# Performance work log

Measured on AMD Instinct MI355X. Metric: run time of the kernel, lower is better.

## Reference

```python
import jax, jax.numpy as jnp
import numpy as np
import math

B, S, D, H = 4, 1024, 1024, 16
DK = D // H


def setup_inputs() -> dict:
    key = jax.random.key(0)
    ks = jax.random.split(key, 13)
    s = 1.0 / math.sqrt(D)
    inp = {
        "query": jax.random.normal(ks[0], (B, S, D), jnp.float32),
        "key": jax.random.normal(ks[1], (B, S, D), jnp.float32),
        "value": jax.random.normal(ks[2], (B, S, D), jnp.float32),
        "mask": jax.random.randint(ks[3], (B, S, S), 0, 2, jnp.int32),
        "wq": jax.random.normal(ks[4], (D, D), jnp.float32) * s,
        "bq": jax.random.normal(ks[5], (D,), jnp.float32) * s,
        "wk": jax.random.normal(ks[6], (D, D), jnp.float32) * s,
        "bk": jax.random.normal(ks[7], (D,), jnp.float32) * s,
        "wv": jax.random.normal(ks[8], (D, D), jnp.float32) * s,
        "bv": jax.random.normal(ks[9], (D,), jnp.float32) * s,
        "wo": jax.random.normal(ks[10], (D, D), jnp.float32) * s,
        "bo": jax.random.normal(ks[11], (D,), jnp.float32) * s,
    }
    return inp


def reference(query, key, value, mask, wq, bq, wk, bk, wv, bv, wo, bo):
    # QKV projections, split into heads: [B,S,D] -> [B,H,S,DK]
    def proj(x, w, b):
        return (x @ w.T + b).reshape(B, S, H, DK).transpose(0, 2, 1, 3)

    q = proj(query, wq, bq)
    k = proj(key, wk, bk)
    v = proj(value, wv, bv)

    scores = jnp.einsum("bhqd,bhkd->bhqk", q, k) / math.sqrt(DK)
    scores = scores + mask[:, None, :, :].astype(scores.dtype) * (-1e9)
    p = jax.nn.softmax(scores, axis=-1)
    x = jnp.einsum("bhqk,bhkd->bhqd", p, v)
    x = x.transpose(0, 2, 1, 3).reshape(B, S, D)
    # output projection (dropout is identity in eval)
    return x @ wo.T + bo
```

## Files before the change

### kernel.cpp

```cpp
#include <hip/hip_runtime.h>
#include <hip/hip_bf16.h>


typedef __bf16 bf16x8 __attribute__((ext_vector_type(8)));
typedef float f32x4 __attribute__((ext_vector_type(4)));
typedef unsigned short us8 __attribute__((ext_vector_type(8)));
typedef unsigned short us4 __attribute__((ext_vector_type(4)));

#define MFMA(a, b, c) __builtin_amdgcn_mfma_f32_16x16x32_bf16(a, b, c, 0, 0, 0)
#define EXP2(x) __builtin_amdgcn_exp2f(x)

__device__ __forceinline__ unsigned short f2b(float f) {
  return __builtin_bit_cast(unsigned short, __float2bfloat16(f));
}
__device__ __forceinline__ float b2f(unsigned short u) {
  return __builtin_bit_cast(float, (unsigned)u << 16);
}
__device__ __forceinline__ unsigned cvtpk(float lo, float hi) {
  unsigned r;
  asm("v_cvt_pk_bf16_f32 %0, %1, %2" : "=v"(r) : "v"(lo), "v"(hi));
  return r;
}
__device__ __forceinline__ bf16x8 ldbf8(const unsigned short* p) {
  return __builtin_bit_cast(bf16x8, *reinterpret_cast<const us8*>(p));
}
__device__ __forceinline__ us8 cvt8(float4 a, float4 b) {
  us8 o;
  o[0] = f2b(a.x); o[1] = f2b(a.y); o[2] = f2b(a.z); o[3] = f2b(a.w);
  o[4] = f2b(b.x); o[5] = f2b(b.y); o[6] = f2b(b.z); o[7] = f2b(b.w);
  return o;
}
__device__ __forceinline__ void glds16(const void* g, void* l) {
  __builtin_amdgcn_global_load_lds(
      (const __attribute__((address_space(1))) unsigned int*)g,
      (__attribute__((address_space(3))) unsigned int*)l, 16, 0, 0);
}

__global__ __launch_bounds__(256)
void prep(const float* __restrict__ query, const float* __restrict__ key,
          const float* __restrict__ value, const float* __restrict__ wq,
          const float* __restrict__ wk, const float* __restrict__ wv,
          unsigned short* __restrict__ Abfq, unsigned short* __restrict__ Abfk,
          unsigned short* __restrict__ Abfv, unsigned short* __restrict__ Wb) {
  const int bid = blockIdx.x, tid = threadIdx.x;
  const float* src;
  unsigned short* dst;
  size_t off;
  if (bid < 1536) {
    const int widx = bid >> 9;
    src = (widx == 0) ? wq : (widx == 1) ? wk : wv;
    dst = Wb + (size_t)widx * 1048576;
    off = (size_t)(bid & 511) * 2048 + tid * 8;
  } else if (bid < 3584) {
    src = query; dst = Abfq; off = (size_t)(bid - 1536) * 2048 + tid * 8;
  } else if (bid < 5632) {
    src = key; dst = Abfk; off = (size_t)(bid - 3584) * 2048 + tid * 8;
  } else {
    src = value; dst = Abfv; off = (size_t)(bid - 5632) * 2048 + tid * 8;
  }
  const float4* p = reinterpret_cast<const float4*>(src + off);
  *reinterpret_cast<us8*>(dst + off) = cvt8(p[0], p[1]);
}

__global__ __launch_bounds__(256)
void maskcvt(const int* __restrict__ mask, unsigned short* __restrict__ Mf) {
  const int idx = blockIdx.x * 256 + threadIdx.x;
  const int wl = idx & 63, tile = idx >> 6;
  const int kt = tile & 63, qt = (tile >> 6) & 63, b = tile >> 12;
  const int lr = wl & 15, lg = wl >> 4;
  const int4 mv = *reinterpret_cast<const int4*>(
      mask + (size_t)(b * 1024 + qt * 16 + lr) * 1024 + kt * 16 + lg * 4);
  us4 o;
  o[0] = mv.x ? 0xCEACu : 0xC1C0u;
  o[1] = mv.y ? 0xCEACu : 0xC1C0u;
  o[2] = mv.z ? 0xCEACu : 0xC1C0u;
  o[3] = mv.w ? 0xCEACu : 0xC1C0u;
  *reinterpret_cast<us4*>(Mf + (size_t)idx * 4) = o;
}

__global__ __launch_bounds__(256)
void cvt_w(const float* __restrict__ src, unsigned short* __restrict__ dst) {
  const size_t off = (size_t)blockIdx.x * 2048 + threadIdx.x * 8;
  const float4* p = reinterpret_cast<const float4*>(src + off);
  *reinterpret_cast<us8*>(dst + off) = cvt8(p[0], p[1]);
}

__global__ __launch_bounds__(256, 4)
void gemm_proj(const unsigned short* __restrict__ Aq,
               const unsigned short* __restrict__ Ak,
               const unsigned short* __restrict__ Av_bf,
               const float* __restrict__ Av_f32,
               const unsigned short* __restrict__ Wb,
               const float* __restrict__ bq, const float* __restrict__ bk,
               const float* __restrict__ bv, unsigned short* __restrict__ Qb,
               unsigned short* __restrict__ Kf, unsigned short* __restrict__ Vf,
               float qscale) {
  constexpr int K = 1024, N = 1024;
  __shared__ __align__(16) unsigned short As[2][128 * 32];
  __shared__ __align__(16) unsigned short Bs[2][128 * 32];
  const int lid = blockIdx.x + (blockIdx.y << 5) + (blockIdx.z << 8);
  const int xcd = lid & 7, slot = lid >> 3;
  const int chunk = ((slot >> 3) << 3) + xcd;
  const int z = chunk >> 5;
  const int bm = (chunk & 31) * 128;
  const int bn = (slot & 7) * 128;

  const unsigned short* Abf = (z == 0) ? Aq : (z == 1) ? Ak : Av_bf;
  const bool f32path = (z == 2) && (Av_bf == nullptr);
  const unsigned short* Bw = Wb + (size_t)z * 1048576;
  const float* bias = (z == 0) ? bq : (z == 1) ? bk : bv;
  const int t = threadIdx.x;
  const int w = t >> 6, lane = t & 63, lr = lane & 15, lg = lane >> 4;
  const int wr = w >> 1, wc = w & 1;

#define SWZ(row) ((((row) ^ ((row) >> 2)) & 3) << 4)

  f32x4 acc[4][4];
#pragma unroll
  for (int m = 0; m < 4; ++m)
#pragma unroll
    for (int n = 0; n < 4; ++n) acc[m][n] = f32x4{0.f, 0.f, 0.f, 0.f};

  auto stageA = [&](int k0, int buf) {
#pragma unroll
    for (int it = 0; it < 2; ++it) {
      const int s = it * 256 + t, row = s >> 2, cb = (s & 3) * 16;
      const char* g = (const char*)Abf + ((size_t)(bm + row) * 1024 + k0) * 2 +
                      (cb ^ SWZ(row));
      char* l = (char*)&As[buf][0] + (it * 256 + w * 64) * 16;
      glds16(g, l);
    }
  };
  auto stageB = [&](int k0, int buf) {
#pragma unroll
    for (int it = 0; it < 2; ++it) {
      const int s = it * 256 + t, row = s >> 2, cb = (s & 3) * 16;
      const char* g = (const char*)Bw + ((size_t)(bn + row) * 1024 + k0) * 2 +
                      (cb ^ SWZ(row));
      char* l = (char*)&Bs[buf][0] + (it * 256 + w * 64) * 16;
      glds16(g, l);
    }
  };
#define STA8(buf, it, v)                                                       \
  {                                                                            \
    const int s_ = (it) * 256 + t, row_ = s_ >> 2, cb_ = (s_ & 3) * 16;        \
    *reinterpret_cast<us8*>((char*)&As[buf][0] + row_ * 64 +                   \
                            (cb_ ^ SWZ(row_))) = (v);                          \
  }

  if (f32path) {
#pragma unroll
    for (int it = 0; it < 2; ++it) {
      const int s = it * 256 + t, row = s >> 2, col = (s & 3) * 8;
      const float4* p =
          reinterpret_cast<const float4*>(Av_f32 + (size_t)(bm + row) * K + col);
      STA8(0, it, cvt8(p[0], p[1]));
    }
  } else {
    stageA(0, 0);
  }
  stageB(0, 0);
  __syncthreads();

  for (int c = 0; c < 32; ++c) {
    const int buf = c & 1;
    float4 fa[4];
    if (c < 31) {
      const int k1 = (c + 1) * 32;
      if (f32path) {
#pragma unroll
        for (int it = 0; it < 2; ++it) {
          const int s = it * 256 + t, row = s >> 2, col = (s & 3) * 8;
          const float4* p = reinterpret_cast<const float4*>(
              Av_f32 + (size_t)(bm + row) * K + k1 + col);
          fa[2 * it] = p[0];
          fa[2 * it + 1] = p[1];
        }
      } else {
        stageA(k1, buf ^ 1);
      }
      stageB(k1, buf ^ 1);
    }
    {
      bf16x8 af[4], bfr[4];
#pragma unroll
      for (int m = 0; m < 4; ++m) {
        const int row = wr * 64 + m * 16 + lr;
        af[m] = ldbf8((const unsigned short*)((char*)&As[buf][0] + row * 64 +
                                              ((lg * 16) ^ SWZ(row))));
      }
#pragma unroll
      for (int n = 0; n < 4; ++n) {
        const int row = wc * 64 + n * 16 + lr;
        bfr[n] = ldbf8((const unsigned short*)((char*)&Bs[buf][0] + row * 64 +
                                               ((lg * 16) ^ SWZ(row))));
      }
#pragma unroll
      for (int m = 0; m < 4; ++m)
#pragma unroll
        for (int n = 0; n < 4; ++n) acc[m][n] = MFMA(af[m], bfr[n], acc[m][n]);
    }
    if (c < 31 && f32path) {
#pragma unroll
      for (int it = 0; it < 2; ++it) STA8(buf ^ 1, it, cvt8(fa[2 * it], fa[2 * it + 1]));
    }
    __syncthreads();
  }
#undef STA8
#undef SWZ

#pragma unroll
  for (int m = 0; m < 4; ++m) {
    const int mr = bm + wr * 64 + m * 16 + lg * 4;
#pragma unroll
    for (int nt = 0; nt < 4; ++nt) {
      const int n = bn + wc * 64 + nt * 16 + lr;
      const float bb = bias[n];
      if (z == 0) {
#pragma unroll
        for (int r = 0; r < 4; ++r)
          Qb[(size_t)(mr + r) * N + n] = f2b((acc[m][nt][r] + bb) * qscale);
      } else if (z == 1) {
        const int b2 = mr >> 10, s0 = mr & 1023, hh = n >> 6, dd = n & 63;
        const size_t base = (size_t)(b2 * 16 + hh) * 65536 + (size_t)(dd >> 5) * 32768 +
                            (size_t)(s0 >> 4) * 512 +
                            (size_t)((s0 & 15) | (((dd >> 3) & 3) << 4)) * 8 + (dd & 7);
#pragma unroll
        for (int r = 0; r < 4; ++r) Kf[base + r * 8] = f2b(acc[m][nt][r] + bb);
      } else {
        const int b2 = mr >> 10, s0 = mr & 1023, hh = n >> 6, dd = n & 63;
        const size_t base = (size_t)(b2 * 16 + hh) * 65536 + (size_t)(s0 >> 5) * 2048 +
                            (size_t)(dd >> 4) * 512 +
                            (size_t)((dd & 15) | (((s0 >> 3) & 3) << 4)) * 8 + (s0 & 7);
        us4 pk;
#pragma unroll
        for (int r = 0; r < 4; ++r) pk[r] = f2b(acc[m][nt][r] + bb);
        *reinterpret_cast<us4*>(&Vf[base]) = pk;
      }
    }
  }
}

__global__ __launch_bounds__(256)
void gemm_out(const unsigned short* __restrict__ A, const unsigned short* __restrict__ Bw,
              const float* __restrict__ bias, float* __restrict__ Out) {
  constexpr int K = 1024, N = 1024;
  __shared__ __align__(16) unsigned short As[2][128 * 64];
  __shared__ __align__(16) unsigned short Bs[2][64 * 64];
  const int lid = blockIdx.x + (blockIdx.y << 5);
  const int xcd = lid & 7, slot = lid >> 3;
  const int chunk = ((slot >> 5) << 3) + xcd;
  const int pos = slot & 31;
  const int bm = ((chunk << 1) + (pos >> 4)) * 128;
  const int bn = (pos & 15) * 64;
  const int t = threadIdx.x;
  const int w = t >> 6, lane = t & 63, lr = lane & 15, lg = lane >> 4;
  const int wr = w >> 1, wc = w & 1;
  const int swzc = (lr & 7) << 4;

  f32x4 acc[4][2];
#pragma unroll
  for (int m = 0; m < 4; ++m)
#pragma unroll
    for (int n = 0; n < 2; ++n) acc[m][n] = f32x4{0.f, 0.f, 0.f, 0.f};

  auto stageA = [&](int k0, int buf) {
#pragma unroll
    for (int it = 0; it < 4; ++it) {
      const int s = it * 256 + t, row = s >> 3, cb = (s & 7) * 16;
      const char* g = (const char*)A + ((size_t)(bm + row) * 1024 + k0) * 2 +
                      (cb ^ ((row & 7) << 4));
      char* l = (char*)&As[buf][0] + (it * 256 + w * 64) * 16;
      glds16(g, l);
    }
  };
  auto stageB = [&](int k0, int buf) {
#pragma unroll
    for (int it = 0; it < 2; ++it) {
      const int s = it * 256 + t, row = s >> 3, cb = (s & 7) * 16;
      const char* g = (const char*)Bw + ((size_t)(bn + row) * 1024 + k0) * 2 +
                      (cb ^ ((row & 7) << 4));
      char* l = (char*)&Bs[buf][0] + (it * 256 + w * 64) * 16;
      glds16(g, l);
    }
  };

  stageA(0, 0);
  stageB(0, 0);
  __syncthreads();

  for (int c = 0; c < 16; ++c) {
    const int buf = c & 1;
    if (c < 15) {
      const int k1 = (c + 1) * 64;
      stageA(k1, buf ^ 1);
      stageB(k1, buf ^ 1);
    }
#pragma unroll
    for (int h2 = 0; h2 < 2; ++h2) {
      bf16x8 af[4], bfr[2];
#pragma unroll
      for (int m = 0; m < 4; ++m) {
        const int row = wr * 64 + m * 16 + lr;
        af[m] = ldbf8((const unsigned short*)((char*)&As[buf][0] + row * 128 +
                                              ((h2 * 64 + lg * 16) ^ swzc)));
      }
#pragma unroll
      for (int n = 0; n < 2; ++n) {
        const int row = wc * 32 + n * 16 + lr;
        bfr[n] = ldbf8((const unsigned short*)((char*)&Bs[buf][0] + row * 128 +
                                               ((h2 * 64 + lg * 16) ^ swzc)));
      }
#pragma unroll
      for (int m = 0; m < 4; ++m)
#pragma unroll
        for (int n = 0; n < 2; ++n) acc[m][n] = MFMA(af[m], bfr[n], acc[m][n]);
    }
    __syncthreads();
  }

#pragma unroll
  for (int m = 0; m < 4; ++m) {
    const int mr = bm + wr * 64 + m * 16 + lg * 4;
#pragma unroll
    for (int nt = 0; nt < 2; ++nt) {
      const int n = bn + wc * 32 + nt * 16 + lr;
      const float bb = bias[n];
#pragma unroll
      for (int r = 0; r < 4; ++r) Out[(size_t)(mr + r) * N + n] = acc[m][nt][r] + bb;
    }
  }
}

__global__ __launch_bounds__(256)
void attn_v6(const unsigned short* __restrict__ Qb,
             const unsigned short* __restrict__ Kf,
             const unsigned short* __restrict__ Vf,
             const unsigned short* __restrict__ Mf,
             unsigned short* __restrict__ ctx) {
  __shared__ __align__(16) unsigned short sP[4][16 * 64];
  const int lid = blockIdx.x + (blockIdx.y << 6);
  const int xcd = lid & 7, slot = lid >> 3;
  const int bh = ((slot >> 4) << 3) + xcd;
  const int qb = slot & 15;
  const int b = bh >> 4, h = bh & 15;
  const int t = threadIdx.x, w = t >> 6, wl = t & 63, lr = wl & 15, lg = wl >> 4;
  const int q0 = qb * 64 + w * 16;
  const int swz = (lr & 7) << 4;

  const unsigned short* qp = Qb + (size_t)(b * 1024 + q0 + lr) * 1024 + h * 64 + lg * 8;
  const bf16x8 bq0 = ldbf8(qp);
  const bf16x8 bq1 = ldbf8(qp + 32);

  const unsigned short* KfB = Kf + (size_t)bh * 65536;
  const unsigned short* VfB = Vf + (size_t)bh * 65536;
  const unsigned short* mfp = Mf + (size_t)((b * 64 + qb * 4 + w) * 64) * 256 + wl * 4;

  f32x4 O[4];
  float l_ = 0.f;
#pragma unroll
  for (int dt = 0; dt < 4; ++dt) O[dt] = f32x4{0.f, 0.f, 0.f, 0.f};
  unsigned short* sp = &sP[w][0];

  for (int kc = 0; kc < 16; ++kc) {
    bf16x8 ak[4][2];
#pragma unroll
    for (int t4 = 0; t4 < 4; ++t4) {
      ak[t4][0] = ldbf8(KfB + (size_t)(kc * 4 + t4) * 512 + wl * 8);
      ak[t4][1] = ldbf8(KfB + 32768 + (size_t)(kc * 4 + t4) * 512 + wl * 8);
    }
    us4 mk[4];
#pragma unroll
    for (int t4 = 0; t4 < 4; ++t4)
      mk[t4] = *reinterpret_cast<const us4*>(mfp + (size_t)(kc * 4 + t4) * 256);
    bf16x8 bv[2][4];
#pragma unroll
    for (int ks = 0; ks < 2; ++ks)
#pragma unroll
      for (int dt = 0; dt < 4; ++dt)
        bv[ks][dt] = ldbf8(VfB + (size_t)(kc * 2 + ks) * 2048 + dt * 512 + wl * 8);

    f32x4 sc[4];
    __builtin_amdgcn_s_setprio(1);
#pragma unroll
    for (int t4 = 0; t4 < 4; ++t4) {
      f32x4 a;
#pragma unroll
      for (int r = 0; r < 4; ++r) a[r] = b2f(mk[t4][r]);
      a = MFMA(ak[t4][0], bq0, a);
      a = MFMA(ak[t4][1], bq1, a);
      sc[t4] = a;
    }
    __builtin_amdgcn_s_setprio(0);

    float ps = 0.f;
#pragma unroll
    for (int t4 = 0; t4 < 4; ++t4) {
      const float e0 = EXP2(sc[t4][0]), e1 = EXP2(sc[t4][1]);
      const float e2 = EXP2(sc[t4][2]), e3 = EXP2(sc[t4][3]);
      ps += (e0 + e1) + (e2 + e3);
      uint2 pw;
      pw.x = cvtpk(e0, e1);
      pw.y = cvtpk(e2, e3);
      *reinterpret_cast<uint2*>((char*)sp + lr * 128 + ((t4 * 32 + lg * 8) ^ swz)) = pw;
    }
    ps += __shfl_xor(ps, 16);
    ps += __shfl_xor(ps, 32);
    l_ += ps;

    __builtin_amdgcn_s_setprio(1);
#pragma unroll
    for (int ks = 0; ks < 2; ++ks) {
      bf16x8 ap =
          ldbf8((const unsigned short*)((char*)sp + lr * 128 + ((ks * 64 + lg * 16) ^ swz)));
#pragma unroll
      for (int dt = 0; dt < 4; ++dt) O[dt] = MFMA(ap, bv[ks][dt], O[dt]);
    }
    __builtin_amdgcn_s_setprio(0);
  }

  float linv[4];
#pragma unroll
  for (int r = 0; r < 4; ++r) linv[r] = 1.0f / __shfl(l_, lg * 4 + r);
#pragma unroll
  for (int dt = 0; dt < 4; ++dt)
#pragma unroll
    for (int r = 0; r < 4; ++r)
      ctx[(size_t)(b * 1024 + q0 + lg * 4 + r) * 1024 + h * 64 + dt * 16 + lr] =
          f2b(O[dt][r] * linv[r]);
}

extern "C" void kernel_launch(void* const* d_in, const int* in_sizes, int n_in,
                              void* d_out, int out_size, void* d_ws, size_t ws_size,
                              hipStream_t stream) {
  const float* query = (const float*)d_in[0];
  const float* key   = (const float*)d_in[1];
  const float* value = (const float*)d_in[2];
  const int*   mask  = (const int*)d_in[3];
  const float* wq = (const float*)d_in[4];
  const float* bq = (const float*)d_in[5];
  const float* wk = (const float*)d_in[6];
  const float* bk = (const float*)d_in[7];
  const float* wv = (const float*)d_in[8];
  const float* bv = (const float*)d_in[9];
  const float* wo = (const float*)d_in[10];
  const float* bo = (const float*)d_in[11];
  float* out = (float*)d_out;

  const size_t SZ = (size_t)4096 * 1024;
  unsigned short* Qb   = (unsigned short*)d_ws;
  unsigned short* Kf   = Qb + SZ;
  unsigned short* Vf   = Kf + SZ;
  unsigned short* ctx  = Vf + SZ;
  unsigned short* Abfq = (unsigned short*)d_out;
  unsigned short* Wb   = Abfq + SZ;
  unsigned short* Mf   = (unsigned short*)d_out;
  unsigned short* Abfk = ctx;
  const bool big = ws_size >= (size_t)40 * 1024 * 1024;
  unsigned short* Abfv = big ? (ctx + SZ) : nullptr;
  unsigned short* Wob  = Vf;

  const float qscale = 0.125f * 1.4426950408889634f;
  dim3 blk(256);
  prep<<<big ? 7680 : 5632, blk, 0, stream>>>(query, key, value, wq, wk, wv,
                                              Abfq, Abfk, Abfv, Wb);
  gemm_proj<<<dim3(32, 8, 3), blk, 0, stream>>>(Abfq, Abfk, Abfv, value, Wb,
                                                bq, bk, bv, Qb, Kf, Vf, qscale);
  maskcvt<<<4096, blk, 0, stream>>>(mask, Mf);
  attn_v6<<<dim3(64, 16), blk, 0, stream>>>(Qb, Kf, Vf, Mf, ctx);
  cvt_w<<<512, blk, 0, stream>>>(wo, Wob);
  gemm_out<<<dim3(32, 16), blk, 0, stream>>>(ctx, Wob, bo, out);
}
```

Before: 123.9 us.

## Stage K/V tiles into double-buffered LDS with async global-to-LDS loads in attention

The attention kernel previously had all four waves load the same K and V fragments straight from global memory into registers. It now stages each key chunk's K and V tiles into a double-buffered shared-memory area using direct global-to-LDS loads, prefetching the next chunk while the current one is computed. This cuts redundant global traffic across the four waves and overlaps loads with compute, at the cost of a block-wide barrier every iteration and more LDS use, which can lower occupancy.

```diff
diff --git a/kernel.cpp b/kernel.cpp
--- a/kernel.cpp
+++ b/kernel.cpp
@@ -333,11 +333,12 @@
 }
 
 __global__ __launch_bounds__(256)
-void attn_v6(const unsigned short* __restrict__ Qb,
+void attn_v7(const unsigned short* __restrict__ Qb,
              const unsigned short* __restrict__ Kf,
              const unsigned short* __restrict__ Vf,
              const unsigned short* __restrict__ Mf,
              unsigned short* __restrict__ ctx) {
+  __shared__ __align__(16) unsigned short S[2][8192];
   __shared__ __align__(16) unsigned short sP[4][16 * 64];
   const int lid = blockIdx.x + (blockIdx.y << 6);
   const int xcd = lid & 7, slot = lid >> 3;
@@ -362,23 +363,35 @@
   for (int dt = 0; dt < 4; ++dt) O[dt] = f32x4{0.f, 0.f, 0.f, 0.f};
   unsigned short* sp = &sP[w][0];
 
+  auto stage = [&](int kc, int buf) {
+    const unsigned short* srcs[4] = {KfB + kc * 2048, KfB + 32768 + kc * 2048,
+                                     VfB + kc * 4096, VfB + kc * 4096 + 2048};
+#pragma unroll
+    for (int r = 0; r < 4; ++r) {
+      const char* g = (const char*)(srcs[r] + (size_t)t * 8);
+      char* l = (char*)&S[buf][r * 2048 + w * 512];
+      glds16(g, l);
+    }
+  };
+
+  stage(0, 0);
+  __syncthreads();
+
   for (int kc = 0; kc < 16; ++kc) {
-    bf16x8 ak[4][2];
-#pragma unroll
-    for (int t4 = 0; t4 < 4; ++t4) {
-      ak[t4][0] = ldbf8(KfB + (size_t)(kc * 4 + t4) * 512 + wl * 8);
-      ak[t4][1] = ldbf8(KfB + 32768 + (size_t)(kc * 4 + t4) * 512 + wl * 8);
-    }
+    const int buf = kc & 1;
+    if (kc < 15) stage(kc + 1, buf ^ 1);
+
     us4 mk[4];
 #pragma unroll
     for (int t4 = 0; t4 < 4; ++t4)
       mk[t4] = *reinterpret_cast<const us4*>(mfp + (size_t)(kc * 4 + t4) * 256);
-    bf16x8 bv[2][4];
-#pragma unroll
-    for (int ks = 0; ks < 2; ++ks)
-#pragma unroll
-      for (int dt = 0; dt < 4; ++dt)
-        bv[ks][dt] = ldbf8(VfB + (size_t)(kc * 2 + ks) * 2048 + dt * 512 + wl * 8);
+
+    bf16x8 ak[4][2];
+#pragma unroll
+    for (int t4 = 0; t4 < 4; ++t4) {
+      ak[t4][0] = ldbf8(&S[buf][t4 * 512 + wl * 8]);
+      ak[t4][1] = ldbf8(&S[buf][2048 + t4 * 512 + wl * 8]);
+    }
 
     f32x4 sc[4];
     __builtin_amdgcn_s_setprio(1);
@@ -414,9 +427,14 @@
       bf16x8 ap =
           ldbf8((const unsigned short*)((char*)sp + lr * 128 + ((ks * 64 + lg * 16) ^ swz)));
 #pragma unroll
-      for (int dt = 0; dt < 4; ++dt) O[dt] = MFMA(ap, bv[ks][dt], O[dt]);
+      for (int dt = 0; dt < 4; ++dt) {
+        bf16x8 bv = ldbf8(&S[buf][4096 + ks * 2048 + dt * 512 + wl * 8]);
+        O[dt] = MFMA(ap, bv, O[dt]);
+      }
     }
     __builtin_amdgcn_s_setprio(0);
+
+    __syncthreads();
   }
 
   float linv[4];
@@ -467,7 +485,7 @@
   gemm_proj<<<dim3(32, 8, 3), blk, 0, stream>>>(Abfq, Abfk, Abfv, value, Wb,
                                                 bq, bk, bv, Qb, Kf, Vf, qscale);
   maskcvt<<<4096, blk, 0, stream>>>(mask, Mf);
-  attn_v6<<<dim3(64, 16), blk, 0, stream>>>(Qb, Kf, Vf, Mf, ctx);
+  attn_v7<<<dim3(64, 16), blk, 0, stream>>>(Qb, Kf, Vf, Mf, ctx);
   cvt_w<<<512, blk, 0, stream>>>(wo, Wob);
   gemm_out<<<dim3(32, 16), blk, 0, stream>>>(ctx, Wob, bo, out);
 }
```

Result: faster. 116.5 us (-6.0%).
